# Kernel tuning notes

Measured on AMD Instinct MI355X. Metric: run time of the kernel, lower is better.

## Reference

```python
import jax, jax.numpy as jnp
import numpy as np

N = 50000   # nodes
E = 500000  # edges
IN = 128    # input_dim
H = 8       # num_heads
D = 32      # hidden_dim (per head)
HD = H * D  # 256
PERM = 100
B = 64      # graphs in batch
C = 10      # num_classes
SLOPE = 0.2 # DGL GATConv leaky_relu default


def setup_inputs() -> dict:
    key = jax.random.key(0)
    ks = jax.random.split(key, 16)
    def glorot(k, shape, fan_in):
        return jax.random.normal(k, shape, dtype=jnp.float32) / np.sqrt(fan_in)
    return {
        "h": jax.random.normal(ks[0], (N, IN), dtype=jnp.float32),
        "perm_features": jax.random.normal(ks[1], (B, PERM), dtype=jnp.float32),
        "W1": glorot(ks[2], (IN, HD), IN),
        "al1": glorot(ks[3], (H, D), D),
        "ar1": glorot(ks[4], (H, D), D),
        "b1": jnp.zeros((HD,), jnp.float32),
        "W2": glorot(ks[5], (HD, HD), HD),
        "al2": glorot(ks[6], (H, D), D),
        "ar2": glorot(ks[7], (H, D), D),
        "b2": jnp.zeros((HD,), jnp.float32),
        "Wc": glorot(ks[8], (HD + PERM, C), HD + PERM),
        "bc": jnp.zeros((C,), jnp.float32),
        "src": jax.random.randint(ks[9], (E,), 0, N, dtype=jnp.int32),
        "dst": jax.random.randint(ks[10], (E,), 0, N, dtype=jnp.int32),
        "graph_ids": jnp.sort(jax.random.randint(ks[11], (N,), 0, B, dtype=jnp.int32)),
    }


def _leaky_relu(x):
    return jnp.where(x > 0, x, SLOPE * x)


def gat_conv(h, W, al, ar, b, src, dst):
    """DGL GATConv: multi-head edge attention + segment softmax + scatter-agg."""
    n = h.shape[0]
    z = (h @ W).reshape(n, H, D)                       # [N,H,D]
    el = jnp.einsum('nhd,hd->nh', z, al)               # [N,H]
    er = jnp.einsum('nhd,hd->nh', z, ar)               # [N,H]
    e = _leaky_relu(el[src] + er[dst])                 # [E,H]
    # segment softmax over incoming edges of each dst node
    m = jax.ops.segment_max(e, dst, num_segments=n)    # [N,H]
    m = jnp.where(jnp.isfinite(m), m, 0.0)             # empty segments -> 0
    w = jnp.exp(e - m[dst])                            # [E,H]
    s = jax.ops.segment_sum(w, dst, num_segments=n)    # [N,H]
    alpha = w / s[dst]                                 # [E,H]
    # weighted scatter-aggregate of source messages
    out = jax.ops.segment_sum(alpha[:, :, None] * z[src], dst, num_segments=n)
    return out + b.reshape(1, H, D)                    # [N,H,D]


def reference(h, perm_features, W1, al1, ar1, b1, W2, al2, ar2, b2, Wc, bc,
              src, dst, graph_ids):
    h1 = jax.nn.relu(gat_conv(h, W1, al1, ar1, b1, src, dst)).reshape(N, HD)
    h2 = gat_conv(h1, W2, al2, ar2, b2, src, dst).reshape(N, HD)
    # dgl.mean_nodes: per-graph mean over nodes
    sums = jax.ops.segment_sum(h2, graph_ids, num_segments=B)            # [B,HD]
    cnts = jax.ops.segment_sum(jnp.ones((N, 1), h2.dtype), graph_ids,
                               num_segments=B)                            # [B,1]
    hg = sums / jnp.maximum(cnts, 1.0)
    combined = jnp.concatenate([hg, perm_features], axis=1)               # [B,HD+PERM]
    return combined @ Wc + bc                                             # [B,C]
```

## Files before the change

kernel.cpp:

```cpp
#include <hip/hip_runtime.h>
#include <hip/hip_bf16.h>

#define NN 50000
#define NE 500000
#define INDIM 128
#define NH 8
#define DH 32
#define HD 256
#define NPERM 100
#define NB_G 64
#define NC 10
#define SLOPE 0.2f
#define BCAP 64

typedef short bf16x8 __attribute__((ext_vector_type(8)));
typedef float f32x4 __attribute__((ext_vector_type(4)));

__device__ inline float bf2f(unsigned short u) {
    union { unsigned int i; float f; } x; x.i = ((unsigned int)u) << 16; return x.f;
}
__device__ inline unsigned short f2bf(float f) {
    __hip_bfloat16 h = __float2bfloat16(f);
    return *reinterpret_cast<unsigned short*>(&h);
}


#define NB_CNT ((NN + 255) / 256)

__global__ __launch_bounds__(256) void prep_kernel(
    int* __restrict__ counts,
    const float* __restrict__ W1, const float* __restrict__ W2,
    __hip_bfloat16* __restrict__ Wt1, __hip_bfloat16* __restrict__ Wt2,
    float* __restrict__ hg)
{
    int b = blockIdx.x;
    int c = threadIdx.x;
    if (b < NB_CNT) {
        int i = b * 256 + c;
        if (i < NN) counts[i] = 0;
    } else {
        int bb = b - NB_CNT;
        if (bb < INDIM) {
            Wt1[(size_t)c * INDIM + bb] = __float2bfloat16(W1[(size_t)bb * HD + c]);
        } else {
            int k = bb - INDIM;
            Wt2[(size_t)c * HD + k] = __float2bfloat16(W2[(size_t)k * HD + c]);
        }
        if (bb < NB_G) hg[bb * HD + c] = 0.f;
    }
}


__global__ __launch_bounds__(256) void scatter_bucket_kernel(
    const int* __restrict__ dst, const int* __restrict__ src,
    int* __restrict__ counts, int* __restrict__ bucket, int ne)
{
    int e = blockIdx.x * 256 + threadIdx.x;
    if (e < ne) {
        int d = dst[e];
        int p = atomicAdd(&counts[d], 1);
        if (p < BCAP) bucket[(size_t)d * BCAP + p] = src[e];
    }
}


template<int IS_F32>
__global__ __launch_bounds__(512) void gemm_mfma_kernel(
    const void* __restrict__ Xv, const __hip_bfloat16* __restrict__ Wt,
    const float* __restrict__ al, const float* __restrict__ ar,
    __hip_bfloat16* __restrict__ zb, float* __restrict__ el, float* __restrict__ er,
    int nrows, int K)
{
    __shared__ __attribute__((aligned(16))) unsigned short Xs[128 * 64];
    int t = threadIdx.x;
    int l = t & 63;
    int wv = t >> 6;
    int wr = wv >> 2;
    int wc = wv & 3;
    int nb = blockIdx.x * 128;
    int wcb = wc * 64;
    int lg = l >> 4;
    int lr = l & 15;

    const short* Wt16 = (const short*)Wt;

    f32x4 acc[4][4];
#pragma unroll
    for (int rb = 0; rb < 4; ++rb)
#pragma unroll
        for (int cf = 0; cf < 4; ++cf) acc[rb][cf] = (f32x4){0.f, 0.f, 0.f, 0.f};

    int srow = t >> 2;
    int sslot = t & 3;
    int g_row0 = t >> 3;
    int g_p0   = t & 7;
    int g_row1 = (t + 512) >> 3;
    int g_p1   = t & 7;

    for (int kc = 0; kc < K; kc += 64) {
        bf16x8 b[2][4];
#pragma unroll
        for (int kh = 0; kh < 2; ++kh)
#pragma unroll
            for (int cf = 0; cf < 4; ++cf) {
                int col = wcb + cf * 16 + lr;
                b[kh][cf] = *(const bf16x8*)&Wt16[(size_t)col * K + kc + kh * 32 + lg * 8];
            }

        if (IS_F32) {
            bf16x8 xv0 = {0,0,0,0,0,0,0,0}, xv1 = {0,0,0,0,0,0,0,0};
            int gr = nb + srow;
            if (gr < nrows) {
                const float* Xf = (const float*)Xv;
                const float* p = &Xf[(size_t)gr * K + kc];
                float4 xa = *(const float4*)&p[sslot * 8];
                float4 xb = *(const float4*)&p[sslot * 8 + 4];
                float4 xc = *(const float4*)&p[(sslot + 4) * 8];
                float4 xd = *(const float4*)&p[(sslot + 4) * 8 + 4];
                xv0[0] = (short)f2bf(xa.x); xv0[1] = (short)f2bf(xa.y);
                xv0[2] = (short)f2bf(xa.z); xv0[3] = (short)f2bf(xa.w);
                xv0[4] = (short)f2bf(xb.x); xv0[5] = (short)f2bf(xb.y);
                xv0[6] = (short)f2bf(xb.z); xv0[7] = (short)f2bf(xb.w);
                xv1[0] = (short)f2bf(xc.x); xv1[1] = (short)f2bf(xc.y);
                xv1[2] = (short)f2bf(xc.z); xv1[3] = (short)f2bf(xc.w);
                xv1[4] = (short)f2bf(xd.x); xv1[5] = (short)f2bf(xd.y);
                xv1[6] = (short)f2bf(xd.z); xv1[7] = (short)f2bf(xd.w);
            }
            __syncthreads();
            *(bf16x8*)&Xs[srow * 64 + ((sslot ^ (srow & 7)) * 8)] = xv0;
            *(bf16x8*)&Xs[srow * 64 + (((sslot + 4) ^ (srow & 7)) * 8)] = xv1;
            __syncthreads();
        } else {
            const short* X16 = (const short*)Xv;
            __syncthreads();
            {
                int q0 = g_p0 ^ (g_row0 & 7);
                int q1 = g_p1 ^ (g_row1 & 7);
                const short* ga0 = &X16[(size_t)(nb + g_row0) * K + kc + q0 * 8];
                const short* ga1 = &X16[(size_t)(nb + g_row1) * K + kc + q1 * 8];
                __builtin_amdgcn_global_load_lds(
                    (const __attribute__((address_space(1))) void*)ga0,
                    (__attribute__((address_space(3))) void*)((char*)Xs + t * 16), 16, 0, 0);
                __builtin_amdgcn_global_load_lds(
                    (const __attribute__((address_space(1))) void*)ga1,
                    (__attribute__((address_space(3))) void*)((char*)Xs + (t + 512) * 16), 16, 0, 0);
            }
            __syncthreads();
        }

        bf16x8 a[2][4];
#pragma unroll
        for (int kh = 0; kh < 2; ++kh)
#pragma unroll
            for (int rb = 0; rb < 4; ++rb) {
                int row = wr * 64 + rb * 16 + lr;
                int slot = (kh * 4 + lg) ^ (row & 7);
                a[kh][rb] = *(const bf16x8*)&Xs[row * 64 + slot * 8];
            }
#pragma unroll
        for (int kh = 0; kh < 2; ++kh)
#pragma unroll
            for (int rb = 0; rb < 4; ++rb)
#pragma unroll
                for (int cf = 0; cf < 4; ++cf)
                    acc[rb][cf] = __builtin_amdgcn_mfma_f32_16x16x32_bf16(a[kh][rb], b[kh][cf], acc[rb][cf], 0, 0, 0);
    }

    float al_c[4], ar_c[4];
#pragma unroll
    for (int cf = 0; cf < 4; ++cf) {
        al_c[cf] = al[wcb + cf * 16 + lr];
        ar_c[cf] = ar[wcb + cf * 16 + lr];
    }

    unsigned short* zu = (unsigned short*)zb;
#pragma unroll
    for (int rb = 0; rb < 4; ++rb) {
        int rbase = nb + wr * 64 + rb * 16 + lg * 4;
#pragma unroll
        for (int j = 0; j < 4; ++j) {
            int r = rbase + j;
            if (r < nrows) {
#pragma unroll
                for (int cf = 0; cf < 4; ++cf)
                    zu[(size_t)r * HD + wcb + cf * 16 + lr] = f2bf(acc[rb][cf][j]);
            }
        }
        float p0[4], p1[4], q0[4], q1[4];
#pragma unroll
        for (int j = 0; j < 4; ++j) {
            p0[j] = acc[rb][0][j] * al_c[0] + acc[rb][1][j] * al_c[1];
            p1[j] = acc[rb][2][j] * al_c[2] + acc[rb][3][j] * al_c[3];
            q0[j] = acc[rb][0][j] * ar_c[0] + acc[rb][1][j] * ar_c[1];
            q1[j] = acc[rb][2][j] * ar_c[2] + acc[rb][3][j] * ar_c[3];
        }
#pragma unroll
        for (int m = 1; m < 16; m <<= 1) {
#pragma unroll
            for (int j = 0; j < 4; ++j) {
                p0[j] += __shfl_xor(p0[j], m);
                p1[j] += __shfl_xor(p1[j], m);
                q0[j] += __shfl_xor(q0[j], m);
                q1[j] += __shfl_xor(q1[j], m);
            }
        }
        if (lr == 0) {
#pragma unroll
            for (int j = 0; j < 4; ++j) {
                int r = rbase + j;
                if (r < nrows) {
                    el[(size_t)r * NH + 2 * wc]     = p0[j];
                    el[(size_t)r * NH + 2 * wc + 1] = p1[j];
                    er[(size_t)r * NH + 2 * wc]     = q0[j];
                    er[(size_t)r * NH + 2 * wc + 1] = q1[j];
                }
            }
        }
    }
}


__global__ __launch_bounds__(256) void agg_kernel(
    const __hip_bfloat16* __restrict__ zb, const float* __restrict__ el, const float* __restrict__ er,
    const float* __restrict__ bias, const int* __restrict__ counts,
    const int* __restrict__ bucket, __hip_bfloat16* __restrict__ out, int nrows, int do_relu)
{
    int wid = (blockIdx.x * 256 + threadIdx.x) >> 6;
    int l = threadIdx.x & 63;
    if (wid >= nrows) return;
    int n = wid;
    int K = counts[n];
    if (K > BCAP) K = BCAP;
    const int* srcs = &bucket[(size_t)n * BCAP];
    const unsigned short* zu = (const unsigned short*)zb;

    int es = l >> 4;
    int li = l & 15;
    int hh = li >> 1;
    float ern = er[(size_t)n * NH + hh];
    int c0 = li * 16;

    float num[16];
#pragma unroll
    for (int j = 0; j < 16; ++j) num[j] = 0.f;
    float den = 0.f;

    for (int kb = 0; kb < K; kb += 4) {
        int k = kb + es;
        if (k < K) {
            int s = srcs[k];
            float v = el[(size_t)s * NH + hh] + ern;
            v = v > 0.f ? v : SLOPE * v;
            float w = __expf(v);
            den += w;
            const unsigned short* zr = &zu[(size_t)s * HD + c0];
            bf16x8 z0 = *(const bf16x8*)&zr[0];
            bf16x8 z1 = *(const bf16x8*)&zr[8];
#pragma unroll
            for (int j = 0; j < 8; ++j) {
                num[j]     += w * bf2f((unsigned short)z0[j]);
                num[8 + j] += w * bf2f((unsigned short)z1[j]);
            }
        }
    }

    den += __shfl_xor(den, 16);
    den += __shfl_xor(den, 32);
#pragma unroll
    for (int j = 0; j < 16; ++j) {
        num[j] += __shfl_xor(num[j], 16);
        num[j] += __shfl_xor(num[j], 32);
    }

    if (es == 0) {
        float inv = (K > 0) ? 1.0f / den : 0.f;
        unsigned short* op = (unsigned short*)out;
        float4 bva = *(const float4*)&bias[c0];
        float4 bvb = *(const float4*)&bias[c0 + 4];
        float4 bvc = *(const float4*)&bias[c0 + 8];
        float4 bvd = *(const float4*)&bias[c0 + 12];
        float bb[16] = {bva.x, bva.y, bva.z, bva.w, bvb.x, bvb.y, bvb.z, bvb.w,
                        bvc.x, bvc.y, bvc.z, bvc.w, bvd.x, bvd.y, bvd.z, bvd.w};
        bf16x8 o0, o1;
#pragma unroll
        for (int j = 0; j < 8; ++j) {
            float v0 = num[j] * inv + bb[j];
            float v1 = num[8 + j] * inv + bb[8 + j];
            if (do_relu) { v0 = fmaxf(v0, 0.f); v1 = fmaxf(v1, 0.f); }
            o0[j] = (short)f2bf(v0);
            o1[j] = (short)f2bf(v1);
        }
        *(bf16x8*)&op[(size_t)n * HD + c0] = o0;
        *(bf16x8*)&op[(size_t)n * HD + c0 + 8] = o1;
    }
}


__global__ __launch_bounds__(256) void graph_sum_kernel(
    const __hip_bfloat16* __restrict__ h2, const int* __restrict__ gids,
    float* __restrict__ hg)
{
    int c = threadIdx.x;
    int n0 = blockIdx.x * 64;
    int n1 = n0 + 64;
    if (n0 >= NN) return;
    if (n1 > NN) n1 = NN;
    const unsigned short* hu = (const unsigned short*)h2;
    float acc = 0.f;
    int cur = gids[n0];
    for (int n = n0; n < n1; ++n) {
        int g = gids[n];
        if (g != cur) {
            atomicAdd(&hg[cur * HD + c], acc);
            acc = 0.f;
            cur = g;
        }
        acc += bf2f(hu[(size_t)n * HD + c]);
    }
    atomicAdd(&hg[cur * HD + c], acc);
}

__global__ void classifier_kernel(const float* __restrict__ hg, const float* __restrict__ perm,
                                  const float* __restrict__ Wc, const float* __restrict__ bc,
                                  const int* __restrict__ gids, float* __restrict__ out) {
    int g = blockIdx.x;
    int c = threadIdx.x;
    if (c >= NC) return;
    int lo = 0, hi = NN;
    while (lo < hi) { int mid = (lo + hi) >> 1; if (gids[mid] < g) lo = mid + 1; else hi = mid; }
    int s0 = lo;
    lo = 0; hi = NN;
    while (lo < hi) { int mid = (lo + hi) >> 1; if (gids[mid] < g + 1) lo = mid + 1; else hi = mid; }
    float cnt = fmaxf((float)(lo - s0), 1.0f);
    float inv = 1.0f / cnt;
    float sg = 0.f;
    for (int k = 0; k < HD; ++k) sg += hg[g * HD + k] * Wc[k * NC + c];
    float s = bc[c] + sg * inv;
    for (int k = 0; k < NPERM; ++k) s += perm[g * NPERM + k] * Wc[(HD + k) * NC + c];
    out[g * NC + c] = s;
}


extern "C" void kernel_launch(void* const* d_in, const int* in_sizes, int n_in,
                              void* d_out, int out_size, void* d_ws, size_t ws_size,
                              hipStream_t stream) {
    const float* h    = (const float*)d_in[0];
    const float* perm = (const float*)d_in[1];
    const float* W1   = (const float*)d_in[2];
    const float* al1  = (const float*)d_in[3];
    const float* ar1  = (const float*)d_in[4];
    const float* b1   = (const float*)d_in[5];
    const float* W2   = (const float*)d_in[6];
    const float* al2  = (const float*)d_in[7];
    const float* ar2  = (const float*)d_in[8];
    const float* b2   = (const float*)d_in[9];
    const float* Wc   = (const float*)d_in[10];
    const float* bc   = (const float*)d_in[11];
    const int* src    = (const int*)d_in[12];
    const int* dst    = (const int*)d_in[13];
    const int* gids   = (const int*)d_in[14];
    float* out = (float*)d_out;

    __hip_bfloat16* zb  = (__hip_bfloat16*)d_ws;
    __hip_bfloat16* h1b = zb + (size_t)NN * HD;
    __hip_bfloat16* Wt1 = h1b + (size_t)NN * HD;
    __hip_bfloat16* Wt2 = Wt1 + (size_t)HD * INDIM;
    float* el = (float*)(Wt2 + (size_t)HD * HD);
    float* er = el + (size_t)NN * NH;
    float* hg = er + (size_t)NN * NH;
    int* counts = (int*)(hg + NB_G * HD);
    int* bucket = counts + NN;

    int nblocks_e = (NE + 255) / 256;

    prep_kernel<<<NB_CNT + INDIM + HD, 256, 0, stream>>>(counts, W1, W2, Wt1, Wt2, hg);
    scatter_bucket_kernel<<<nblocks_e, 256, 0, stream>>>(dst, src, counts, bucket, NE);

    int gemm_blocks = (NN + 127) / 128;
    int wave_node_blocks = (NN * 64 + 255) / 256;

    gemm_mfma_kernel<1><<<gemm_blocks, 512, 0, stream>>>(h, Wt1, al1, ar1, zb, el, er, NN, INDIM);
    agg_kernel<<<wave_node_blocks, 256, 0, stream>>>(zb, el, er, b1, counts, bucket, h1b, NN, 1);
    gemm_mfma_kernel<0><<<gemm_blocks, 512, 0, stream>>>(h1b, Wt2, al2, ar2, zb, el, er, NN, HD);
    agg_kernel<<<wave_node_blocks, 256, 0, stream>>>(zb, el, er, b2, counts, bucket, h1b, NN, 0);

    graph_sum_kernel<<<(NN + 63) / 64, 256, 0, stream>>>(h1b, gids, hg);
    classifier_kernel<<<NB_G, 64, 0, stream>>>(hg, perm, Wc, bc, gids, out);
}
```

Before: 227.4 us.

## Fuse edge bucketing into first GEMM launch and shrink GEMM tile to 64 rows

```diff
diff --git a/kernel.cpp b/kernel.cpp
--- a/kernel.cpp
+++ b/kernel.cpp
@@ -51,33 +51,31 @@
 }
 
 
-__global__ __launch_bounds__(256) void scatter_bucket_kernel(
-    const int* __restrict__ dst, const int* __restrict__ src,
-    int* __restrict__ counts, int* __restrict__ bucket, int ne)
-{
-    int e = blockIdx.x * 256 + threadIdx.x;
-    if (e < ne) {
-        int d = dst[e];
-        int p = atomicAdd(&counts[d], 1);
-        if (p < BCAP) bucket[(size_t)d * BCAP + p] = src[e];
-    }
-}
-
-
 template<int IS_F32>
-__global__ __launch_bounds__(512) void gemm_mfma_kernel(
+__global__ __launch_bounds__(256) void gemm_mfma_kernel(
     const void* __restrict__ Xv, const __hip_bfloat16* __restrict__ Wt,
     const float* __restrict__ al, const float* __restrict__ ar,
     __hip_bfloat16* __restrict__ zb, float* __restrict__ el, float* __restrict__ er,
-    int nrows, int K)
+    int nrows, int K, int gemm_nblocks,
+    const int* __restrict__ dstv, const int* __restrict__ srcv,
+    int* __restrict__ counts, int* __restrict__ bucket, int ne)
 {
-    __shared__ __attribute__((aligned(16))) unsigned short Xs[128 * 64];
+    __shared__ __attribute__((aligned(16))) unsigned short Xs[64 * 64];
     int t = threadIdx.x;
+
+    if ((int)blockIdx.x >= gemm_nblocks) {
+        int e = ((int)blockIdx.x - gemm_nblocks) * 256 + t;
+        if (e < ne) {
+            int d = dstv[e];
+            int p = atomicAdd(&counts[d], 1);
+            if (p < BCAP) bucket[(size_t)d * BCAP + p] = srcv[e];
+        }
+        return;
+    }
+
     int l = t & 63;
-    int wv = t >> 6;
-    int wr = wv >> 2;
-    int wc = wv & 3;
-    int nb = blockIdx.x * 128;
+    int wc = t >> 6;
+    int nb = blockIdx.x * 64;
     int wcb = wc * 64;
     int lg = l >> 4;
     int lr = l & 15;
@@ -93,9 +91,8 @@
     int srow = t >> 2;
     int sslot = t & 3;
     int g_row0 = t >> 3;
-    int g_p0   = t & 7;
-    int g_row1 = (t + 512) >> 3;
-    int g_p1   = t & 7;
+    int g_row1 = (t + 256) >> 3;
+    int g_p    = t & 7;
 
     for (int kc = 0; kc < K; kc += 64) {
         bf16x8 b[2][4];
@@ -134,8 +131,8 @@
             const short* X16 = (const short*)Xv;
             __syncthreads();
             {
-                int q0 = g_p0 ^ (g_row0 & 7);
-                int q1 = g_p1 ^ (g_row1 & 7);
+                int q0 = g_p ^ (g_row0 & 7);
+                int q1 = g_p ^ (g_row1 & 7);
                 const short* ga0 = &X16[(size_t)(nb + g_row0) * K + kc + q0 * 8];
                 const short* ga1 = &X16[(size_t)(nb + g_row1) * K + kc + q1 * 8];
                 __builtin_amdgcn_global_load_lds(
@@ -143,7 +140,7 @@
                     (__attribute__((address_space(3))) void*)((char*)Xs + t * 16), 16, 0, 0);
                 __builtin_amdgcn_global_load_lds(
                     (const __attribute__((address_space(1))) void*)ga1,
-                    (__attribute__((address_space(3))) void*)((char*)Xs + (t + 512) * 16), 16, 0, 0);
+                    (__attribute__((address_space(3))) void*)((char*)Xs + (t + 256) * 16), 16, 0, 0);
             }
             __syncthreads();
         }
@@ -153,7 +150,7 @@
         for (int kh = 0; kh < 2; ++kh)
 #pragma unroll
             for (int rb = 0; rb < 4; ++rb) {
-                int row = wr * 64 + rb * 16 + lr;
+                int row = rb * 16 + lr;
                 int slot = (kh * 4 + lg) ^ (row & 7);
                 a[kh][rb] = *(const bf16x8*)&Xs[row * 64 + slot * 8];
             }
@@ -176,7 +173,7 @@
     unsigned short* zu = (unsigned short*)zb;
 #pragma unroll
     for (int rb = 0; rb < 4; ++rb) {
-        int rbase = nb + wr * 64 + rb * 16 + lg * 4;
+        int rbase = nb + rb * 16 + lg * 4;
 #pragma unroll
         for (int j = 0; j < 4; ++j) {
             int r = rbase + j;
@@ -372,16 +369,18 @@
     int* bucket = counts + NN;
 
     int nblocks_e = (NE + 255) / 256;
+    int gemm_blocks = (NN + 63) / 64;
+    int wave_node_blocks = (NN * 64 + 255) / 256;
 
     prep_kernel<<<NB_CNT + INDIM + HD, 256, 0, stream>>>(counts, W1, W2, Wt1, Wt2, hg);
-    scatter_bucket_kernel<<<nblocks_e, 256, 0, stream>>>(dst, src, counts, bucket, NE);
-
-    int gemm_blocks = (NN + 127) / 128;
-    int wave_node_blocks = (NN * 64 + 255) / 256;
-
-    gemm_mfma_kernel<1><<<gemm_blocks, 512, 0, stream>>>(h, Wt1, al1, ar1, zb, el, er, NN, INDIM);
+
+    gemm_mfma_kernel<1><<<gemm_blocks + nblocks_e, 256, 0, stream>>>(
+        h, Wt1, al1, ar1, zb, el, er, NN, INDIM,
+        gemm_blocks, dst, src, counts, bucket, NE);
     agg_kernel<<<wave_node_blocks, 256, 0, stream>>>(zb, el, er, b1, counts, bucket, h1b, NN, 1);
-    gemm_mfma_kernel<0><<<gemm_blocks, 512, 0, stream>>>(h1b, Wt2, al2, ar2, zb, el, er, NN, HD);
+    gemm_mfma_kernel<0><<<gemm_blocks, 256, 0, stream>>>(
+        h1b, Wt2, al2, ar2, zb, el, er, NN, HD,
+        gemm_blocks, nullptr, nullptr, nullptr, nullptr, 0);
     agg_kernel<<<wave_node_blocks, 256, 0, stream>>>(zb, el, er, b2, counts, bucket, h1b, NN, 0);
 
     graph_sum_kernel<<<(NN + 63) / 64, 256, 0, stream>>>(h1b, gids, hg);
```

After: 212.1 us. -6.7%, faster.
